# Optimization experiments

Measured on AMD Instinct MI355X. Metric: run time of the kernel, lower is better.

Reference implementation:

```python
import jax, jax.numpy as jnp
import numpy as np

NUM_QUBITS = 12
NUM_LAYERS = 2
STATE_DIM = 2 ** NUM_QUBITS
BATCH = 4096
TWO_PI = 2 * 3.1416  # matches the original initializer constant


def _u3(theta, phi, lam):
    """Single-qubit U3 gate, 2x2 complex64 (matches TF layer exactly)."""
    c = jnp.cos(theta / 2)
    s = jnp.sin(theta / 2)
    z = jnp.zeros_like(phi)
    e_phi = jnp.exp(jax.lax.complex(z, phi))
    e_lam = jnp.exp(jax.lax.complex(z, lam))
    e_pl = jnp.exp(jax.lax.complex(z, phi + lam))
    cc = jax.lax.complex(c, jnp.zeros_like(c))
    sc = jax.lax.complex(s, jnp.zeros_like(s))
    row1 = jnp.stack([cc, -e_lam * sc])
    row2 = jnp.stack([e_phi * sc, e_pl * cc])
    return jnp.stack([row1, row2])  # [2, 2] complex64


def _full_gate(theta_vec, phi_vec, lam_vec):
    """Kronecker product of per-qubit gates -> [2^n, 2^n] complex64."""
    full = _u3(theta_vec[0], phi_vec[0], lam_vec[0])
    for q in range(1, theta_vec.shape[0]):
        full = jnp.kron(full, _u3(theta_vec[q], phi_vec[q], lam_vec[q]))
    return full


def setup_inputs() -> dict:
    key = jax.random.key(0)
    k1, k2, k3, k4 = jax.random.split(key, 4)
    inputs = jax.random.normal(k1, (BATCH, STATE_DIM), dtype=jnp.float32)
    thetas = jax.random.uniform(k2, (NUM_LAYERS, NUM_QUBITS), minval=0.0, maxval=TWO_PI, dtype=jnp.float32)
    phis = jax.random.uniform(k3, (NUM_LAYERS, NUM_QUBITS), minval=0.0, maxval=TWO_PI, dtype=jnp.float32)
    lams = jax.random.uniform(k4, (NUM_LAYERS, NUM_QUBITS), minval=0.0, maxval=TWO_PI, dtype=jnp.float32)
    return {"inputs": inputs, "thetas": thetas, "phis": phis, "lams": lams}


def reference(inputs, thetas, phis, lams):
    # normalize real inputs as complex state, per-sample L2 norm
    state = jax.lax.complex(inputs, jnp.zeros_like(inputs))  # [B, D] complex64
    norm = jnp.linalg.norm(state, axis=1, keepdims=True)      # real, [B, 1]
    state = state / norm
    for l in range(thetas.shape[0]):
        U = _full_gate(thetas[l], phis[l], lams[l])  # [D, D]
        # matvec(U, x) per sample == state @ U^T, batched GEMM replaces tf.map_fn
        state = state @ U.T
    return jnp.real(state * jnp.conj(state))  # probabilities, [B, D] float32
```

## Files before the change

### kernel.cpp

```cpp
#include <hip/hip_runtime.h>

#define NQ   12
#define DIM  4096
#define NL   2
#define BATCH 4096

typedef float v2f __attribute__((ext_vector_type(2)));


struct PGate { v2f a00, b00, a01, b01, a10, b10, a11, b11; };

__device__ __forceinline__ PGate make_pg(const float* __restrict__ g) {
    PGate p;
    float r00 = g[0], i00 = g[1], r01 = g[2], i01 = g[3];
    float r10 = g[4], i10 = g[5], r11 = g[6], i11 = g[7];
    p.a00 = (v2f){ r00, i00 };  p.b00 = (v2f){ -i00, r00 };
    p.a01 = (v2f){ r01, i01 };  p.b01 = (v2f){ -i01, r01 };
    p.a10 = (v2f){ r10, i10 };  p.b10 = (v2f){ -i10, r10 };
    p.a11 = (v2f){ r11, i11 };  p.b11 = (v2f){ -i11, r11 };
    return p;
}

__device__ __forceinline__ void papply(v2f v[16], int r0, int r1, const PGate& g) {
    v2f x0 = v[r0], x1 = v[r1];
    v2f x0r = (v2f){ x0.x, x0.x }, x0i = (v2f){ x0.y, x0.y };
    v2f x1r = (v2f){ x1.x, x1.x }, x1i = (v2f){ x1.y, x1.y };
    v[r0] = g.a00 * x0r + g.b00 * x0i + g.a01 * x1r + g.b01 * x1i;
    v[r1] = g.a10 * x0r + g.b10 * x0i + g.a11 * x1r + g.b11 * x1i;
}

__device__ __forceinline__ void papply_rbit(v2f v[16], int rb, const PGate& g) {
    const int m = 1 << rb;
    #pragma unroll
    for (int h = 0; h < 8; ++h) {
        int low = h & (m - 1);
        int r   = ((h & ~(m - 1)) << 1) | low;
        papply(v, r, r | m, g);
    }
}

__device__ __forceinline__ int lds_off(int idx) { return idx + (idx >> 4); }

__global__ __launch_bounds__(256, 4)
void qc_sim(const float* __restrict__ in,
            const float* __restrict__ th,
            const float* __restrict__ ph,
            const float* __restrict__ lm,
            float* __restrict__ out) {
    __shared__ v2f   st[DIM + DIM / 16];
    __shared__ float sg[NQ][8];
    __shared__ float red[4];

    const int t = threadIdx.x;
    const int b = blockIdx.x;

    v2f v[16];
    float ss = 0.f;

    const float4* __restrict__ x4 =
        reinterpret_cast<const float4*>(in + (size_t)b * DIM);
    #pragma unroll
    for (int j = 0; j < 4; ++j) {
        float4 w = x4[j * 256 + t];
        int r = j * 4;
        v[r]     = (v2f){ w.x, 0.f };
        v[r + 1] = (v2f){ w.y, 0.f };
        v[r + 2] = (v2f){ w.z, 0.f };
        v[r + 3] = (v2f){ w.w, 0.f };
        ss += w.x * w.x + w.y * w.y + w.z * w.z + w.w * w.w;
    }
    #pragma unroll
    for (int off = 32; off > 0; off >>= 1)
        ss += __shfl_down(ss, off, 64);
    if ((t & 63) == 0) red[t >> 6] = ss;

    if (t < NQ) {
        int q = t;
        float g00r = 1.f, g00i = 0.f, g01r = 0.f, g01i = 0.f;
        float g10r = 0.f, g10i = 0.f, g11r = 1.f, g11i = 0.f;
        #pragma unroll
        for (int l = 0; l < NL; ++l) {
            float th2 = 0.5f * th[l * NQ + q];
            float p   = ph[l * NQ + q];
            float la  = lm[l * NQ + q];
            float c = cosf(th2), s = sinf(th2);
            float u00r = c,                u00i = 0.f;
            float u01r = -cosf(la) * s,    u01i = -sinf(la) * s;
            float u10r = cosf(p) * s,      u10i = sinf(p) * s;
            float u11r = cosf(p + la) * c, u11i = sinf(p + la) * c;
            float n00r = u00r*g00r - u00i*g00i + u01r*g10r - u01i*g10i;
            float n00i = u00r*g00i + u00i*g00r + u01r*g10i + u01i*g10r;
            float n01r = u00r*g01r - u00i*g01i + u01r*g11r - u01i*g11i;
            float n01i = u00r*g01i + u00i*g01r + u01r*g11i + u01i*g11r;
            float n10r = u10r*g00r - u10i*g00i + u11r*g10r - u11i*g10i;
            float n10i = u10r*g00i + u10i*g00r + u11r*g10i + u11i*g10r;
            float n11r = u10r*g01r - u10i*g01i + u11r*g11r - u11i*g11i;
            float n11i = u10r*g01i + u10i*g01r + u11r*g11i + u11i*g11r;
            g00r = n00r; g00i = n00i; g01r = n01r; g01i = n01i;
            g10r = n10r; g10i = n10i; g11r = n11r; g11i = n11i;
        }
        int k = (NQ - 1) - q;
        sg[k][0] = g00r; sg[k][1] = g00i; sg[k][2] = g01r; sg[k][3] = g01i;
        sg[k][4] = g10r; sg[k][5] = g10i; sg[k][6] = g11r; sg[k][7] = g11i;
    }
    __syncthreads();

    {
        PGate g0 = make_pg(sg[0]);
        #pragma unroll
        for (int r = 0; r < 16; r += 2) {
            v2f x0r = (v2f){ v[r].x,     v[r].x     };
            v2f x1r = (v2f){ v[r + 1].x, v[r + 1].x };
            v[r]     = g0.a00 * x0r + g0.a01 * x1r;
            v[r + 1] = g0.a10 * x0r + g0.a11 * x1r;
        }
        { PGate g = make_pg(sg[1]);  papply_rbit(v, 1, g); }
        { PGate g = make_pg(sg[10]); papply_rbit(v, 2, g); }
        { PGate g = make_pg(sg[11]); papply_rbit(v, 3, g); }
    }
    #pragma unroll
    for (int r = 0; r < 16; ++r) {
        int idx = ((r >> 2) << 10) + t * 4 + (r & 3);
        st[lds_off(idx)] = v[r];
    }
    __syncthreads();

    #pragma unroll
    for (int r = 0; r < 16; ++r) {
        int idx = ((t >> 2) << 6) + (r << 2) + (t & 3);
        v[r] = st[lds_off(idx)];
    }
    { PGate g = make_pg(sg[2]); papply_rbit(v, 0, g); }
    { PGate g = make_pg(sg[3]); papply_rbit(v, 1, g); }
    { PGate g = make_pg(sg[4]); papply_rbit(v, 2, g); }
    { PGate g = make_pg(sg[5]); papply_rbit(v, 3, g); }
    __syncthreads();
    #pragma unroll
    for (int r = 0; r < 16; ++r) {
        int idx = ((t >> 2) << 6) + (r << 2) + (t & 3);
        st[lds_off(idx)] = v[r];
    }
    __syncthreads();

    #pragma unroll
    for (int r = 0; r < 16; ++r) {
        int idx = ((t >> 6) << 10) + (r << 6) + (t & 63);
        v[r] = st[lds_off(idx)];
    }
    { PGate g = make_pg(sg[6]); papply_rbit(v, 0, g); }
    { PGate g = make_pg(sg[7]); papply_rbit(v, 1, g); }
    { PGate g = make_pg(sg[8]); papply_rbit(v, 2, g); }
    { PGate g = make_pg(sg[9]); papply_rbit(v, 3, g); }

    float tot = red[0] + red[1] + red[2] + red[3];
    float inv = 1.0f / tot;
    float* __restrict__ o = out + (size_t)b * DIM;
    #pragma unroll
    for (int r = 0; r < 16; ++r) {
        int idx = ((t >> 6) << 10) + (r << 6) + (t & 63);
        v2f p2 = v[r] * v[r];
        o[idx] = (p2.x + p2.y) * inv;
    }
}

extern "C" void kernel_launch(void* const* d_in, const int* in_sizes, int n_in,
                              void* d_out, int out_size, void* d_ws, size_t ws_size,
                              hipStream_t stream) {
    (void)in_sizes; (void)n_in; (void)out_size; (void)d_ws; (void)ws_size;
    const float* inputs = (const float*)d_in[0];
    const float* thetas = (const float*)d_in[1];
    const float* phis   = (const float*)d_in[2];
    const float* lams   = (const float*)d_in[3];
    float* out = (float*)d_out;

    hipLaunchKernelGGL(qc_sim, dim3(BATCH), dim3(256), 0, stream,
                       inputs, thetas, phis, lams, out);
}
```

Before: 137.4 us.

## Process two samples per block, interleaving LDS transposes with gate math

Each block now handles two batch samples and launches half as many blocks. The LDS transpose of one sample alternates with the gate math of the other, so synchronisation and LDS latency can be hidden behind arithmetic. Gate coefficients are now computed redundantly by every wave, which removes the barrier before the first gate stage, and the sin/cos calls use fast __sincosf intrinsics. The cost is double the register state per thread, which may lower occupancy, plus extra barriers per block and an unsynchronised read of shared gate data that relies on ordering within a wave.

```diff
diff --git a/kernel.cpp b/kernel.cpp
--- a/kernel.cpp
+++ b/kernel.cpp
@@ -21,10 +21,12 @@
     return p;
 }
 
+__device__ __forceinline__ v2f blo(v2f x) { return __builtin_shufflevector(x, x, 0, 0); }
+__device__ __forceinline__ v2f bhi(v2f x) { return __builtin_shufflevector(x, x, 1, 1); }
+
 __device__ __forceinline__ void papply(v2f v[16], int r0, int r1, const PGate& g) {
     v2f x0 = v[r0], x1 = v[r1];
-    v2f x0r = (v2f){ x0.x, x0.x }, x0i = (v2f){ x0.y, x0.y };
-    v2f x1r = (v2f){ x1.x, x1.x }, x1i = (v2f){ x1.y, x1.y };
+    v2f x0r = blo(x0), x0i = bhi(x0), x1r = blo(x1), x1i = bhi(x1);
     v[r0] = g.a00 * x0r + g.b00 * x0i + g.a01 * x1r + g.b01 * x1i;
     v[r1] = g.a10 * x0r + g.b10 * x0i + g.a11 * x1r + g.b11 * x1i;
 }
@@ -40,6 +42,23 @@
 }
 
 __device__ __forceinline__ int lds_off(int idx) { return idx + (idx >> 4); }
+
+__device__ __forceinline__ int idxW1(int r, int t) { return ((r >> 2) << 10) + (t << 2) + (r & 3); }
+__device__ __forceinline__ int idxS2(int r, int t) { return ((t >> 2) << 6) + (r << 2) + (t & 3); }
+__device__ __forceinline__ int idxS3(int r, int t) { return ((t >> 6) << 10) + (r << 6) + (t & 63); }
+
+__device__ __forceinline__ void math_s2(v2f v[16], float sg[NQ][8]) {
+    { PGate g = make_pg(sg[2]); papply_rbit(v, 0, g); }
+    { PGate g = make_pg(sg[3]); papply_rbit(v, 1, g); }
+    { PGate g = make_pg(sg[4]); papply_rbit(v, 2, g); }
+    { PGate g = make_pg(sg[5]); papply_rbit(v, 3, g); }
+}
+__device__ __forceinline__ void math_s3(v2f v[16], float sg[NQ][8]) {
+    { PGate g = make_pg(sg[6]); papply_rbit(v, 0, g); }
+    { PGate g = make_pg(sg[7]); papply_rbit(v, 1, g); }
+    { PGate g = make_pg(sg[8]); papply_rbit(v, 2, g); }
+    { PGate g = make_pg(sg[9]); papply_rbit(v, 3, g); }
+}
 
 __global__ __launch_bounds__(256, 4)
 void qc_sim(const float* __restrict__ in,
@@ -49,33 +68,25 @@
             float* __restrict__ out) {
     __shared__ v2f   st[DIM + DIM / 16];
     __shared__ float sg[NQ][8];
-    __shared__ float red[4];
-
-    const int t = threadIdx.x;
-    const int b = blockIdx.x;
-
-    v2f v[16];
-    float ss = 0.f;
-
-    const float4* __restrict__ x4 =
-        reinterpret_cast<const float4*>(in + (size_t)b * DIM);
-    #pragma unroll
-    for (int j = 0; j < 4; ++j) {
-        float4 w = x4[j * 256 + t];
-        int r = j * 4;
-        v[r]     = (v2f){ w.x, 0.f };
-        v[r + 1] = (v2f){ w.y, 0.f };
-        v[r + 2] = (v2f){ w.z, 0.f };
-        v[r + 3] = (v2f){ w.w, 0.f };
-        ss += w.x * w.x + w.y * w.y + w.z * w.z + w.w * w.w;
-    }
-    #pragma unroll
-    for (int off = 32; off > 0; off >>= 1)
-        ss += __shfl_down(ss, off, 64);
-    if ((t & 63) == 0) red[t >> 6] = ss;
-
-    if (t < NQ) {
-        int q = t;
+    __shared__ float red[8];
+
+    const int t    = threadIdx.x;
+    const int lane = t & 63;
+    const int b    = blockIdx.x;
+
+    const size_t baseA = (size_t)(2 * b) * DIM;
+    const size_t baseB = baseA + DIM;
+
+    const float4* __restrict__ xA = reinterpret_cast<const float4*>(in + baseA);
+    const float4* __restrict__ xB = reinterpret_cast<const float4*>(in + baseB);
+    float4 lA[4], lB[4];
+    #pragma unroll
+    for (int j = 0; j < 4; ++j) lA[j] = xA[j * 256 + t];
+    #pragma unroll
+    for (int j = 0; j < 4; ++j) lB[j] = xB[j * 256 + t];
+
+    if (lane < NQ) {
+        int q = lane;
         float g00r = 1.f, g00i = 0.f, g01r = 0.f, g01i = 0.f;
         float g10r = 0.f, g10i = 0.f, g11r = 1.f, g11i = 0.f;
         #pragma unroll
@@ -83,11 +94,15 @@
             float th2 = 0.5f * th[l * NQ + q];
             float p   = ph[l * NQ + q];
             float la  = lm[l * NQ + q];
-            float c = cosf(th2), s = sinf(th2);
-            float u00r = c,                u00i = 0.f;
-            float u01r = -cosf(la) * s,    u01i = -sinf(la) * s;
-            float u10r = cosf(p) * s,      u10i = sinf(p) * s;
-            float u11r = cosf(p + la) * c, u11i = sinf(p + la) * c;
+            float s, c, sl, cl, sp, cp, spl, cpl;
+            __sincosf(th2, &s, &c);
+            __sincosf(la, &sl, &cl);
+            __sincosf(p, &sp, &cp);
+            __sincosf(p + la, &spl, &cpl);
+            float u00r = c,        u00i = 0.f;
+            float u01r = -cl * s,  u01i = -sl * s;
+            float u10r = cp * s,   u10i = sp * s;
+            float u11r = cpl * c,  u11i = spl * c;
             float n00r = u00r*g00r - u00i*g00i + u01r*g10r - u01i*g10i;
             float n00i = u00r*g00i + u00i*g00r + u01r*g10i + u01i*g10r;
             float n01r = u00r*g01r - u00i*g01i + u01r*g11r - u01i*g11i;
@@ -103,63 +118,87 @@
         sg[k][0] = g00r; sg[k][1] = g00i; sg[k][2] = g01r; sg[k][3] = g01i;
         sg[k][4] = g10r; sg[k][5] = g10i; sg[k][6] = g11r; sg[k][7] = g11i;
     }
-    __syncthreads();
+
+    float ssA = 0.f, ssB = 0.f;
+    #pragma unroll
+    for (int j = 0; j < 4; ++j) {
+        ssA += lA[j].x*lA[j].x + lA[j].y*lA[j].y + lA[j].z*lA[j].z + lA[j].w*lA[j].w;
+        ssB += lB[j].x*lB[j].x + lB[j].y*lB[j].y + lB[j].z*lB[j].z + lB[j].w*lB[j].w;
+    }
+    #pragma unroll
+    for (int off = 32; off > 0; off >>= 1) {
+        ssA += __shfl_down(ssA, off, 64);
+        ssB += __shfl_down(ssB, off, 64);
+    }
+    if (lane == 0) { red[t >> 6] = ssA; red[4 + (t >> 6)] = ssB; }
+
+    v2f vA[16], vB[16];
 
     {
-        PGate g0 = make_pg(sg[0]);
-        #pragma unroll
-        for (int r = 0; r < 16; r += 2) {
-            v2f x0r = (v2f){ v[r].x,     v[r].x     };
-            v2f x1r = (v2f){ v[r + 1].x, v[r + 1].x };
-            v[r]     = g0.a00 * x0r + g0.a01 * x1r;
-            v[r + 1] = g0.a10 * x0r + g0.a11 * x1r;
-        }
-        { PGate g = make_pg(sg[1]);  papply_rbit(v, 1, g); }
-        { PGate g = make_pg(sg[10]); papply_rbit(v, 2, g); }
-        { PGate g = make_pg(sg[11]); papply_rbit(v, 3, g); }
-    }
-    #pragma unroll
-    for (int r = 0; r < 16; ++r) {
-        int idx = ((r >> 2) << 10) + t * 4 + (r & 3);
-        st[lds_off(idx)] = v[r];
-    }
-    __syncthreads();
-
-    #pragma unroll
-    for (int r = 0; r < 16; ++r) {
-        int idx = ((t >> 2) << 6) + (r << 2) + (t & 3);
-        v[r] = st[lds_off(idx)];
-    }
-    { PGate g = make_pg(sg[2]); papply_rbit(v, 0, g); }
-    { PGate g = make_pg(sg[3]); papply_rbit(v, 1, g); }
-    { PGate g = make_pg(sg[4]); papply_rbit(v, 2, g); }
-    { PGate g = make_pg(sg[5]); papply_rbit(v, 3, g); }
-    __syncthreads();
-    #pragma unroll
-    for (int r = 0; r < 16; ++r) {
-        int idx = ((t >> 2) << 6) + (r << 2) + (t & 3);
-        st[lds_off(idx)] = v[r];
-    }
-    __syncthreads();
-
-    #pragma unroll
-    for (int r = 0; r < 16; ++r) {
-        int idx = ((t >> 6) << 10) + (r << 6) + (t & 63);
-        v[r] = st[lds_off(idx)];
-    }
-    { PGate g = make_pg(sg[6]); papply_rbit(v, 0, g); }
-    { PGate g = make_pg(sg[7]); papply_rbit(v, 1, g); }
-    { PGate g = make_pg(sg[8]); papply_rbit(v, 2, g); }
-    { PGate g = make_pg(sg[9]); papply_rbit(v, 3, g); }
-
-    float tot = red[0] + red[1] + red[2] + red[3];
-    float inv = 1.0f / tot;
-    float* __restrict__ o = out + (size_t)b * DIM;
-    #pragma unroll
-    for (int r = 0; r < 16; ++r) {
-        int idx = ((t >> 6) << 10) + (r << 6) + (t & 63);
-        v2f p2 = v[r] * v[r];
-        o[idx] = (p2.x + p2.y) * inv;
+        v2f c00 = (v2f){ sg[0][0], sg[0][1] }, c01 = (v2f){ sg[0][2], sg[0][3] };
+        v2f c10 = (v2f){ sg[0][4], sg[0][5] }, c11 = (v2f){ sg[0][6], sg[0][7] };
+        #pragma unroll
+        for (int j = 0; j < 4; ++j) {
+            v2f x0, x1;
+            x0 = (v2f){ lA[j].x, lA[j].x }; x1 = (v2f){ lA[j].y, lA[j].y };
+            vA[4*j]   = c00 * x0 + c01 * x1;  vA[4*j+1] = c10 * x0 + c11 * x1;
+            x0 = (v2f){ lA[j].z, lA[j].z }; x1 = (v2f){ lA[j].w, lA[j].w };
+            vA[4*j+2] = c00 * x0 + c01 * x1;  vA[4*j+3] = c10 * x0 + c11 * x1;
+            x0 = (v2f){ lB[j].x, lB[j].x }; x1 = (v2f){ lB[j].y, lB[j].y };
+            vB[4*j]   = c00 * x0 + c01 * x1;  vB[4*j+1] = c10 * x0 + c11 * x1;
+            x0 = (v2f){ lB[j].z, lB[j].z }; x1 = (v2f){ lB[j].w, lB[j].w };
+            vB[4*j+2] = c00 * x0 + c01 * x1;  vB[4*j+3] = c10 * x0 + c11 * x1;
+        }
+        { PGate g = make_pg(sg[1]);  papply_rbit(vA, 1, g); papply_rbit(vB, 1, g); }
+        { PGate g = make_pg(sg[10]); papply_rbit(vA, 2, g); papply_rbit(vB, 2, g); }
+        { PGate g = make_pg(sg[11]); papply_rbit(vA, 3, g); papply_rbit(vB, 3, g); }
+    }
+
+    #pragma unroll
+    for (int r = 0; r < 16; ++r) st[lds_off(idxW1(r, t))] = vA[r];
+    __syncthreads();
+    #pragma unroll
+    for (int r = 0; r < 16; ++r) vA[r] = st[lds_off(idxS2(r, t))];
+    __syncthreads();
+    #pragma unroll
+    for (int r = 0; r < 16; ++r) st[lds_off(idxW1(r, t))] = vB[r];
+    __syncthreads();
+    #pragma unroll
+    for (int r = 0; r < 16; ++r) vB[r] = st[lds_off(idxS2(r, t))];
+    math_s2(vA, sg);
+    __syncthreads();
+    #pragma unroll
+    for (int r = 0; r < 16; ++r) st[lds_off(idxS2(r, t))] = vA[r];
+    __syncthreads();
+    #pragma unroll
+    for (int r = 0; r < 16; ++r) vA[r] = st[lds_off(idxS3(r, t))];
+    math_s2(vB, sg);
+    __syncthreads();
+    #pragma unroll
+    for (int r = 0; r < 16; ++r) st[lds_off(idxS2(r, t))] = vB[r];
+    __syncthreads();
+    #pragma unroll
+    for (int r = 0; r < 16; ++r) vB[r] = st[lds_off(idxS3(r, t))];
+    math_s3(vA, sg);
+
+    {
+        float inv = 1.0f / (red[0] + red[1] + red[2] + red[3]);
+        float* __restrict__ o = out + baseA;
+        #pragma unroll
+        for (int r = 0; r < 16; ++r) {
+            v2f p2 = vA[r] * vA[r];
+            o[idxS3(r, t)] = (p2.x + p2.y) * inv;
+        }
+    }
+    math_s3(vB, sg);
+    {
+        float inv = 1.0f / (red[4] + red[5] + red[6] + red[7]);
+        float* __restrict__ o = out + baseB;
+        #pragma unroll
+        for (int r = 0; r < 16; ++r) {
+            v2f p2 = vB[r] * vB[r];
+            o[idxS3(r, t)] = (p2.x + p2.y) * inv;
+        }
     }
 }
 
@@ -173,6 +212,6 @@
     const float* lams   = (const float*)d_in[3];
     float* out = (float*)d_out;
 
-    hipLaunchKernelGGL(qc_sim, dim3(BATCH), dim3(256), 0, stream,
+    hipLaunchKernelGGL(qc_sim, dim3(BATCH / 2), dim3(256), 0, stream,
                        inputs, thetas, phis, lams, out);
 }
```

Measured after the change: 133.8 us. 1.03x faster.

## Make first LDS transpose wave-local to drop most block barriers

Applied to the files above, without the earlier changes.

Changes the index mapping of the middle stage so each wave reads back only the LDS elements it wrote itself. This lets the first transpose and the gate-matrix setup skip block-wide barriers, going from four __syncthreads to one. Every wave now computes the fused gate matrices redundantly instead of only the first 12 threads, and the trig calls switch to fast __sincosf. Correctness now depends on the wave-ownership property of the new mapping and on in-order LDS visibility within a wave.

```diff
diff --git a/kernel.cpp b/kernel.cpp
--- a/kernel.cpp
+++ b/kernel.cpp
@@ -21,10 +21,12 @@
     return p;
 }
 
+__device__ __forceinline__ v2f blo(v2f x) { return __builtin_shufflevector(x, x, 0, 0); }
+__device__ __forceinline__ v2f bhi(v2f x) { return __builtin_shufflevector(x, x, 1, 1); }
+
 __device__ __forceinline__ void papply(v2f v[16], int r0, int r1, const PGate& g) {
     v2f x0 = v[r0], x1 = v[r1];
-    v2f x0r = (v2f){ x0.x, x0.x }, x0i = (v2f){ x0.y, x0.y };
-    v2f x1r = (v2f){ x1.x, x1.x }, x1i = (v2f){ x1.y, x1.y };
+    v2f x0r = blo(x0), x0i = bhi(x0), x1r = blo(x1), x1i = bhi(x1);
     v[r0] = g.a00 * x0r + g.b00 * x0i + g.a01 * x1r + g.b01 * x1i;
     v[r1] = g.a10 * x0r + g.b10 * x0i + g.a11 * x1r + g.b11 * x1i;
 }
@@ -41,6 +43,17 @@
 
 __device__ __forceinline__ int lds_off(int idx) { return idx + (idx >> 4); }
 
+__device__ __forceinline__ int map1(int r, int t) {
+    return ((r >> 2) << 10) | (t << 2) | (r & 3);
+}
+__device__ __forceinline__ int map2(int r, int t) {
+    return (t & 3) | ((r & 3) << 2) | (((r >> 2) & 3) << 4)
+         | (((t >> 2) & 3) << 6) | (((t >> 6) & 3) << 8) | (((t >> 4) & 3) << 10);
+}
+__device__ __forceinline__ int map3(int r, int t) {
+    return (t & 63) | (r << 6) | ((t >> 6) << 10);
+}
+
 __global__ __launch_bounds__(256, 4)
 void qc_sim(const float* __restrict__ in,
             const float* __restrict__ th,
@@ -51,31 +64,18 @@
     __shared__ float sg[NQ][8];
     __shared__ float red[4];
 
-    const int t = threadIdx.x;
-    const int b = blockIdx.x;
-
-    v2f v[16];
-    float ss = 0.f;
+    const int t    = threadIdx.x;
+    const int lane = t & 63;
+    const int b    = blockIdx.x;
 
     const float4* __restrict__ x4 =
         reinterpret_cast<const float4*>(in + (size_t)b * DIM);
+    float4 lA[4];
     #pragma unroll
-    for (int j = 0; j < 4; ++j) {
-        float4 w = x4[j * 256 + t];
-        int r = j * 4;
-        v[r]     = (v2f){ w.x, 0.f };
-        v[r + 1] = (v2f){ w.y, 0.f };
-        v[r + 2] = (v2f){ w.z, 0.f };
-        v[r + 3] = (v2f){ w.w, 0.f };
-        ss += w.x * w.x + w.y * w.y + w.z * w.z + w.w * w.w;
-    }
-    #pragma unroll
-    for (int off = 32; off > 0; off >>= 1)
-        ss += __shfl_down(ss, off, 64);
-    if ((t & 63) == 0) red[t >> 6] = ss;
+    for (int j = 0; j < 4; ++j) lA[j] = x4[j * 256 + t];
 
-    if (t < NQ) {
-        int q = t;
+    if (lane < NQ) {
+        int q = lane;
         float g00r = 1.f, g00i = 0.f, g01r = 0.f, g01i = 0.f;
         float g10r = 0.f, g10i = 0.f, g11r = 1.f, g11i = 0.f;
         #pragma unroll
@@ -83,11 +83,15 @@
             float th2 = 0.5f * th[l * NQ + q];
             float p   = ph[l * NQ + q];
             float la  = lm[l * NQ + q];
-            float c = cosf(th2), s = sinf(th2);
-            float u00r = c,                u00i = 0.f;
-            float u01r = -cosf(la) * s,    u01i = -sinf(la) * s;
-            float u10r = cosf(p) * s,      u10i = sinf(p) * s;
-            float u11r = cosf(p + la) * c, u11i = sinf(p + la) * c;
+            float s, c, sl, cl, sp, cp, spl, cpl;
+            __sincosf(th2, &s, &c);
+            __sincosf(la, &sl, &cl);
+            __sincosf(p, &sp, &cp);
+            __sincosf(p + la, &spl, &cpl);
+            float u00r = c,        u00i = 0.f;
+            float u01r = -cl * s,  u01i = -sl * s;
+            float u10r = cp * s,   u10i = sp * s;
+            float u11r = cpl * c,  u11i = spl * c;
             float n00r = u00r*g00r - u00i*g00i + u01r*g10r - u01i*g10i;
             float n00i = u00r*g00i + u00i*g00r + u01r*g10i + u01i*g10r;
             float n01r = u00r*g01r - u00i*g01i + u01r*g11r - u01i*g11i;
@@ -103,63 +107,61 @@
         sg[k][0] = g00r; sg[k][1] = g00i; sg[k][2] = g01r; sg[k][3] = g01i;
         sg[k][4] = g10r; sg[k][5] = g10i; sg[k][6] = g11r; sg[k][7] = g11i;
     }
-    __syncthreads();
+
+    float ss = 0.f;
+    #pragma unroll
+    for (int j = 0; j < 4; ++j)
+        ss += lA[j].x*lA[j].x + lA[j].y*lA[j].y + lA[j].z*lA[j].z + lA[j].w*lA[j].w;
+    #pragma unroll
+    for (int off = 32; off > 0; off >>= 1)
+        ss += __shfl_down(ss, off, 64);
+    if (lane == 0) red[t >> 6] = ss;
+
+    v2f v[16];
 
     {
-        PGate g0 = make_pg(sg[0]);
+        v2f c00 = (v2f){ sg[0][0], sg[0][1] }, c01 = (v2f){ sg[0][2], sg[0][3] };
+        v2f c10 = (v2f){ sg[0][4], sg[0][5] }, c11 = (v2f){ sg[0][6], sg[0][7] };
         #pragma unroll
-        for (int r = 0; r < 16; r += 2) {
-            v2f x0r = (v2f){ v[r].x,     v[r].x     };
-            v2f x1r = (v2f){ v[r + 1].x, v[r + 1].x };
-            v[r]     = g0.a00 * x0r + g0.a01 * x1r;
-            v[r + 1] = g0.a10 * x0r + g0.a11 * x1r;
+        for (int j = 0; j < 4; ++j) {
+            v2f x0, x1;
+            x0 = (v2f){ lA[j].x, lA[j].x }; x1 = (v2f){ lA[j].y, lA[j].y };
+            v[4*j]   = c00 * x0 + c01 * x1;  v[4*j+1] = c10 * x0 + c11 * x1;
+            x0 = (v2f){ lA[j].z, lA[j].z }; x1 = (v2f){ lA[j].w, lA[j].w };
+            v[4*j+2] = c00 * x0 + c01 * x1;  v[4*j+3] = c10 * x0 + c11 * x1;
         }
         { PGate g = make_pg(sg[1]);  papply_rbit(v, 1, g); }
         { PGate g = make_pg(sg[10]); papply_rbit(v, 2, g); }
         { PGate g = make_pg(sg[11]); papply_rbit(v, 3, g); }
     }
-    #pragma unroll
-    for (int r = 0; r < 16; ++r) {
-        int idx = ((r >> 2) << 10) + t * 4 + (r & 3);
-        st[lds_off(idx)] = v[r];
-    }
-    __syncthreads();
 
     #pragma unroll
-    for (int r = 0; r < 16; ++r) {
-        int idx = ((t >> 2) << 6) + (r << 2) + (t & 3);
-        v[r] = st[lds_off(idx)];
-    }
+    for (int r = 0; r < 16; ++r) st[lds_off(map1(r, t))] = v[r];
+    #pragma unroll
+    for (int r = 0; r < 16; ++r) v[r] = st[lds_off(map2(r, t))];
+
     { PGate g = make_pg(sg[2]); papply_rbit(v, 0, g); }
     { PGate g = make_pg(sg[3]); papply_rbit(v, 1, g); }
     { PGate g = make_pg(sg[4]); papply_rbit(v, 2, g); }
     { PGate g = make_pg(sg[5]); papply_rbit(v, 3, g); }
+
+    #pragma unroll
+    for (int r = 0; r < 16; ++r) st[lds_off(map2(r, t))] = v[r];
     __syncthreads();
     #pragma unroll
-    for (int r = 0; r < 16; ++r) {
-        int idx = ((t >> 2) << 6) + (r << 2) + (t & 3);
-        st[lds_off(idx)] = v[r];
-    }
-    __syncthreads();
+    for (int r = 0; r < 16; ++r) v[r] = st[lds_off(map3(r, t))];
 
-    #pragma unroll
-    for (int r = 0; r < 16; ++r) {
-        int idx = ((t >> 6) << 10) + (r << 6) + (t & 63);
-        v[r] = st[lds_off(idx)];
-    }
     { PGate g = make_pg(sg[6]); papply_rbit(v, 0, g); }
     { PGate g = make_pg(sg[7]); papply_rbit(v, 1, g); }
     { PGate g = make_pg(sg[8]); papply_rbit(v, 2, g); }
     { PGate g = make_pg(sg[9]); papply_rbit(v, 3, g); }
 
-    float tot = red[0] + red[1] + red[2] + red[3];
-    float inv = 1.0f / tot;
+    float inv = 1.0f / (red[0] + red[1] + red[2] + red[3]);
     float* __restrict__ o = out + (size_t)b * DIM;
     #pragma unroll
     for (int r = 0; r < 16; ++r) {
-        int idx = ((t >> 6) << 10) + (r << 6) + (t & 63);
         v2f p2 = v[r] * v[r];
-        o[idx] = (p2.x + p2.y) * inv;
+        o[map3(r, t)] = (p2.x + p2.y) * inv;
     }
 }
 
```

Result: faster. 133.6 us (-2.8%).
